# Kernel optimization log

Measured on AMD Instinct MI355X. Metric: run time of the kernel, lower is better.

## Reference

```python
import jax, jax.numpy as jnp
import numpy as np

EMBED_DIM = 1024
NUM_HEADS = 16
HEAD_DIM = EMBED_DIM // NUM_HEADS


def setup_inputs() -> dict:
    key = jax.random.key(0)
    ks = jax.random.split(key, 9)
    B, S, D = 2, 2048, EMBED_DIM
    scale = 1.0 / np.sqrt(D)
    x = jax.random.normal(ks[0], (B, S, D), dtype=jnp.float32)
    Wq = jax.random.normal(ks[1], (D, D), dtype=jnp.float32) * scale
    Wk = jax.random.normal(ks[2], (D, D), dtype=jnp.float32) * scale
    Wv = jax.random.normal(ks[3], (D, D), dtype=jnp.float32) * scale
    Wo = jax.random.normal(ks[4], (D, D), dtype=jnp.float32) * scale
    bq = jnp.zeros((D,), jnp.float32)
    bk = jnp.zeros((D,), jnp.float32)
    bv = jnp.zeros((D,), jnp.float32)
    bo = jnp.zeros((D,), jnp.float32)
    return {"x": x, "Wq": Wq, "bq": bq, "Wk": Wk, "bk": bk,
            "Wv": Wv, "bv": bv, "Wo": Wo, "bo": bo}


def reference(x, Wq, bq, Wk, bk, Wv, bv, Wo, bo):
    B, S, D = x.shape
    H, Dh = NUM_HEADS, HEAD_DIM
    # QKV projections -> [B, H, S, Dh]
    q = (x @ Wq + bq).reshape(B, S, H, Dh).transpose(0, 2, 1, 3)
    k = (x @ Wk + bk).reshape(B, S, H, Dh).transpose(0, 2, 1, 3)
    v = (x @ Wv + bv).reshape(B, S, H, Dh).transpose(0, 2, 1, 3)
    # scores [B, H, S, S], scaled by sqrt(head_dim)
    scores = jnp.einsum('bhqd,bhkd->bhqk', q, k) / jnp.sqrt(jnp.float32(Dh))
    attn = jax.nn.softmax(scores, axis=-1)
    out = jnp.einsum('bhqk,bhkd->bhqd', attn, v)  # [B, H, S, Dh]
    out = out.transpose(0, 2, 1, 3).reshape(B, S, D)
    return out @ Wo + bo
```

## Files before the change

### kernel.cpp

```cpp
#include <hip/hip_runtime.h>
#include <hip/hip_bf16.h>

typedef short bf16x8 __attribute__((ext_vector_type(8)));
typedef float f32x4 __attribute__((ext_vector_type(4)));

#define MFMA16(a, b, c) __builtin_amdgcn_mfma_f32_16x16x32_bf16((a), (b), (c), 0, 0, 0)

static constexpr int B_ = 2, S_ = 2048, D_ = 1024, H_ = 16, DH = 64;
static constexpr int M_ = B_ * S_;
static constexpr int K_ = D_;

static __device__ __forceinline__ ushort f2bf(float f) {
    __hip_bfloat16 h = __float2bfloat16(f);
    return *reinterpret_cast<ushort*>(&h);
}

static __device__ __forceinline__ void gload16(const ushort* g, ushort* l) {
    __builtin_amdgcn_global_load_lds((const __attribute__((address_space(1))) void*)g,
                                     (__attribute__((address_space(3))) void*)l, 16, 0, 0);
}

__global__ __launch_bounds__(256) void cvt_f2b(const float* __restrict__ in,
                                               ushort* __restrict__ out) {
    int i = blockIdx.x * blockDim.x + threadIdx.x;
    float4 v = reinterpret_cast<const float4*>(in)[i];
    ushort4 o;
    o.x = f2bf(v.x); o.y = f2bf(v.y); o.z = f2bf(v.z); o.w = f2bf(v.w);
    reinterpret_cast<ushort4*>(out)[i] = o;
}

__global__ __launch_bounds__(256) void transpose_w4(const float* __restrict__ W0,
                                                    const float* __restrict__ W1,
                                                    const float* __restrict__ W2,
                                                    const float* __restrict__ W3,
                                                    ushort* __restrict__ T0,
                                                    ushort* __restrict__ T1,
                                                    ushort* __restrict__ T2,
                                                    ushort* __restrict__ T3) {
    __shared__ float tile[32][33];
    int z = blockIdx.z;
    const float* W = (z == 0) ? W0 : (z == 1) ? W1 : (z == 2) ? W2 : W3;
    ushort* T = (z == 0) ? T0 : (z == 1) ? T1 : (z == 2) ? T2 : T3;
    int bx = blockIdx.x, by = blockIdx.y;
    int tx = threadIdx.x, ty = threadIdx.y;
#pragma unroll
    for (int i = 0; i < 4; i++)
        tile[ty + i * 8][tx] = W[(by * 32 + ty + i * 8) * D_ + bx * 32 + tx];
    __syncthreads();
#pragma unroll
    for (int i = 0; i < 4; i++)
        T[(bx * 32 + ty + i * 8) * K_ + by * 32 + tx] = f2bf(tile[tx][ty + i * 8]);
}

template <int MODE, int TN>
__global__ __launch_bounds__(256, 3) void gemm128(const ushort* __restrict__ A,
                                                  const ushort* __restrict__ Wt,
                                                  const float* __restrict__ bias_q,
                                                  const float* __restrict__ bias_k,
                                                  const float* __restrict__ bias_v,
                                                  ushort* __restrict__ Qb,
                                                  ushort* __restrict__ Kb,
                                                  ushort* __restrict__ Vtb,
                                                  float* __restrict__ outf) {
    constexpr int NJ = TN / 32;
    __shared__ __align__(16) ushort As[128 * 32];
    __shared__ __align__(16) ushort Bs[TN * 32];

    int m0 = blockIdx.x * 128;
    int n0 = blockIdx.y * TN;
    int t = threadIdx.x;
    int lane = t & 63, w = t >> 6;
    int ln = lane & 15, lq = lane >> 4;
    int wm = (w >> 1) * 64, wn = (w & 1) * (TN / 2);

    int c0 = t, c1 = t + 256;
    const ushort* Ag0 = A + (size_t)(m0 + (c0 >> 2)) * K_ + (c0 & 3) * 8;
    const ushort* Ag1 = A + (size_t)(m0 + (c1 >> 2)) * K_ + (c1 & 3) * 8;
    const ushort* Bg0 = Wt + (size_t)(n0 + (c0 >> 2)) * K_ + (c0 & 3) * 8;
    const ushort* Bg1 = Wt + (size_t)(n0 + (c1 >> 2)) * K_ + (c1 & 3) * 8;
    ushort* Al0 = As + c0 * 8;
    ushort* Al1 = As + c1 * 8;
    ushort* Bl0 = Bs + c0 * 8;
    ushort* Bl1 = Bs + c1 * 8;

    f32x4 acc[4][NJ];
#pragma unroll
    for (int i = 0; i < 4; i++)
#pragma unroll
        for (int j = 0; j < NJ; j++) acc[i][j] = f32x4{0.f, 0.f, 0.f, 0.f};

    for (int k0 = 0; k0 < K_; k0 += 32) {
        gload16(Ag0 + k0, Al0);
        gload16(Ag1 + k0, Al1);
        gload16(Bg0 + k0, Bl0);
        if (TN == 128) gload16(Bg1 + k0, Bl1);
        __syncthreads();
        bf16x8 af[4], bfr[NJ];
#pragma unroll
        for (int i = 0; i < 4; i++)
            af[i] = *reinterpret_cast<const bf16x8*>(As + (wm + i * 16 + ln) * 32 + lq * 8);
#pragma unroll
        for (int j = 0; j < NJ; j++)
            bfr[j] = *reinterpret_cast<const bf16x8*>(Bs + (wn + j * 16 + ln) * 32 + lq * 8);
#pragma unroll
        for (int i = 0; i < 4; i++)
#pragma unroll
            for (int j = 0; j < NJ; j++)
                acc[i][j] = MFMA16(af[i], bfr[j], acc[i][j]);
        __syncthreads();
    }

#pragma unroll
    for (int j = 0; j < NJ; j++) {
        int n = n0 + wn + j * 16 + ln;
        if (MODE == 1) {
            float bv = bias_q[n];
#pragma unroll
            for (int i = 0; i < 4; i++) {
#pragma unroll
                for (int r = 0; r < 4; r++) {
                    int m = m0 + wm + i * 16 + lq * 4 + r;
                    outf[(size_t)m * D_ + n] = acc[i][j][r] + bv;
                }
            }
        } else {
            int which = n >> 10, nn = n & 1023, h = nn >> 6, dh = nn & 63;
            const float* bp = (which == 0) ? bias_q : (which == 1) ? bias_k : bias_v;
            float bv = bp[nn];
            if (which == 2) {
#pragma unroll
                for (int i = 0; i < 4; i++) {
                    int m = m0 + wm + i * 16 + lq * 4;
                    int b = m >> 11, s0 = m & 2047;
                    ushort4 o4;
                    o4.x = f2bf(acc[i][j][0] + bv);
                    o4.y = f2bf(acc[i][j][1] + bv);
                    o4.z = f2bf(acc[i][j][2] + bv);
                    o4.w = f2bf(acc[i][j][3] + bv);
                    *reinterpret_cast<ushort4*>(Vtb + (((size_t)(b * H_ + h) * DH) + dh) * S_ + s0) = o4;
                }
            } else {
                ushort* dst = (which == 0) ? Qb : Kb;
#pragma unroll
                for (int i = 0; i < 4; i++) {
#pragma unroll
                    for (int r = 0; r < 4; r++) {
                        int m = m0 + wm + i * 16 + lq * 4 + r;
                        int b = m >> 11, s = m & 2047;
                        dst[(((b * H_ + h) * S_) + s) * DH + dh] = f2bf(acc[i][j][r] + bv);
                    }
                }
            }
        }
    }
}

__global__ __launch_bounds__(256, 4) void attn32d(const ushort* __restrict__ Q,
                                                  const ushort* __restrict__ K,
                                                  const ushort* __restrict__ Vt,
                                                  ushort* __restrict__ O) {
    __shared__ __align__(16) ushort Kl[2][2048];
    __shared__ __align__(16) ushort Vl[2][2048];
    __shared__ __align__(16) short Pl[4][16 * 36];

    int bid = blockIdx.x;
    int qb = bid & 31;
    int bh = bid >> 5;
    int t = threadIdx.x;
    int lane = t & 63, w = t >> 6;
    int ln = lane & 15, lq = lane >> 4;
    int qt = qb * 4 + w;

    const ushort* Qp = Q + (size_t)bh * S_ * DH;
    const ushort* Kp = K + (size_t)bh * S_ * DH;
    const ushort* Vp = Vt + (size_t)bh * DH * S_;

    bf16x8 qf0 = *reinterpret_cast<const bf16x8*>(Qp + (qt * 16 + ln) * DH + lq * 8);
    bf16x8 qf1 = *reinterpret_cast<const bf16x8*>(Qp + (qt * 16 + ln) * DH + 32 + lq * 8);

    const ushort* Kg = Kp + (size_t)(t & 31) * DH + (t >> 5) * 8;
    const ushort* Vg = Vp + (size_t)(t & 63) * S_ + (t >> 6) * 8;

    f32x4 o_acc[4];
    float l_part[4] = {0.f, 0.f, 0.f, 0.f};
#pragma unroll
    for (int nt = 0; nt < 4; nt++) o_acc[nt] = f32x4{0.f, 0.f, 0.f, 0.f};

    gload16(Kg, Kl[0] + t * 8);
    gload16(Vg, Vl[0] + t * 8);

    const float kSc = 0.18033688011112042f;

    for (int kt = 0; kt < S_ / 32; kt++) {
        __syncthreads();
        int cur = kt & 1;
        if (kt + 1 < S_ / 32) {
            int kb = (kt + 1) * 32;
            gload16(Kg + (size_t)kb * DH, Kl[cur ^ 1] + t * 8);
            gload16(Vg + kb, Vl[cur ^ 1] + t * 8);
        }
        const ushort* Kc = Kl[cur];
        const ushort* Vc = Vl[cur];

        f32x4 sc[2];
#pragma unroll
        for (int nt = 0; nt < 2; nt++) {
            bf16x8 kf0 = *reinterpret_cast<const bf16x8*>(Kc + (lq * 32 + nt * 16 + ln) * 8);
            bf16x8 kf1 = *reinterpret_cast<const bf16x8*>(Kc + ((4 + lq) * 32 + nt * 16 + ln) * 8);
            f32x4 c = {0.f, 0.f, 0.f, 0.f};
            c = MFMA16(qf0, kf0, c);
            c = MFMA16(qf1, kf1, c);
            sc[nt] = c;
        }
#pragma unroll
        for (int nt = 0; nt < 2; nt++)
#pragma unroll
            for (int r = 0; r < 4; r++) {
                float p = exp2f(sc[nt][r] * kSc);
                l_part[r] += p;
                Pl[w][(lq * 4 + r) * 36 + nt * 16 + ln] = (short)f2bf(p);
            }
        bf16x8 pf = *reinterpret_cast<const bf16x8*>(&Pl[w][ln * 36 + lq * 8]);
#pragma unroll
        for (int nt = 0; nt < 4; nt++) {
            bf16x8 vf = *reinterpret_cast<const bf16x8*>(Vc + (lq * 64 + nt * 16 + ln) * 8);
            o_acc[nt] = MFMA16(pf, vf, o_acc[nt]);
        }
    }

    float linv[4];
#pragma unroll
    for (int r = 0; r < 4; r++) {
        float l = l_part[r];
#pragma unroll
        for (int d = 1; d < 16; d <<= 1) l += __shfl_xor(l, d, 64);
        linv[r] = 1.0f / l;
    }
    int b = bh >> 4, h = bh & 15;
#pragma unroll
    for (int nt = 0; nt < 4; nt++)
#pragma unroll
        for (int r = 0; r < 4; r++) {
            int s = qt * 16 + lq * 4 + r;
            O[((b * S_ + s) * H_ + h) * DH + nt * 16 + ln] =
                f2bf(o_acc[nt][r] * linv[r]);
        }
}

extern "C" void kernel_launch(void* const* d_in, const int* in_sizes, int n_in,
                              void* d_out, int out_size, void* d_ws, size_t ws_size,
                              hipStream_t stream) {
    const float* x  = (const float*)d_in[0];
    const float* Wq = (const float*)d_in[1];
    const float* bq = (const float*)d_in[2];
    const float* Wk = (const float*)d_in[3];
    const float* bk = (const float*)d_in[4];
    const float* Wv = (const float*)d_in[5];
    const float* bv = (const float*)d_in[6];
    const float* Wo = (const float*)d_in[7];
    const float* bo = (const float*)d_in[8];
    float* out = (float*)d_out;

    char* ws = (char*)d_ws;
    const size_t MB = 1024 * 1024;
    ushort* wtq = (ushort*)(ws + 0 * MB);
    ushort* wtk = (ushort*)(ws + 2 * MB);
    ushort* wtv = (ushort*)(ws + 4 * MB);
    ushort* wto = (ushort*)(ws + 6 * MB);
    ushort* xb  = (ushort*)(ws + 8 * MB);
    ushort* Qb  = (ushort*)(ws + 16 * MB);
    ushort* Kb  = (ushort*)(ws + 24 * MB);
    ushort* Vtb = (ushort*)(ws + 32 * MB);
    ushort* AO  = (ushort*)(ws + 40 * MB);

    cvt_f2b<<<(M_ * K_ / 4) / 256, 256, 0, stream>>>(x, xb);

    transpose_w4<<<dim3(32, 32, 4), dim3(32, 8), 0, stream>>>(
        Wq, Wk, Wv, Wo, wtq, wtk, wtv, wto);

    gemm128<0, 128><<<dim3(M_ / 128, 3072 / 128), 256, 0, stream>>>(
        xb, wtq, bq, bk, bv, Qb, Kb, Vtb, nullptr);

    attn32d<<<32 * 32, 256, 0, stream>>>(Qb, Kb, Vtb, AO);

    gemm128<1, 64><<<dim3(M_ / 128, D_ / 64), 256, 0, stream>>>(
        AO, wto, bo, nullptr, nullptr, nullptr, nullptr, nullptr, out);
}
```

Measured before the change: 214.6 us.

## Split attention over two key halves and merge partial outputs in a combine kernel

The attention kernel now launches twice as many blocks, each covering half of the keys. Each block writes a normalized partial output plus its row sum, and a new combine kernel merges the two halves weighted by those sums. The softmax scale (with log2e folded in) is also moved into the Q weights and bias so the inner loop skips one multiply. This trades an extra kernel launch, partial-output traffic and an extra bf16 rounding for more parallelism in the attention stage. There is still no max subtraction, so it relies on scores staying small enough for exp2 not to overflow.

```diff
diff --git a/kernel.cpp b/kernel.cpp
--- a/kernel.cpp
+++ b/kernel.cpp
@@ -9,10 +9,16 @@
 static constexpr int B_ = 2, S_ = 2048, D_ = 1024, H_ = 16, DH = 64;
 static constexpr int M_ = B_ * S_;
 static constexpr int K_ = D_;
+static constexpr float kQS = 0.18033688011112042f;
 
 static __device__ __forceinline__ ushort f2bf(float f) {
     __hip_bfloat16 h = __float2bfloat16(f);
     return *reinterpret_cast<ushort*>(&h);
+}
+static __device__ __forceinline__ float bf2f(ushort u) {
+    __hip_bfloat16 h;
+    *reinterpret_cast<ushort*>(&h) = u;
+    return __bfloat162float(h);
 }
 
 static __device__ __forceinline__ void gload16(const ushort* g, ushort* l) {
@@ -41,6 +47,7 @@
     int z = blockIdx.z;
     const float* W = (z == 0) ? W0 : (z == 1) ? W1 : (z == 2) ? W2 : W3;
     ushort* T = (z == 0) ? T0 : (z == 1) ? T1 : (z == 2) ? T2 : T3;
+    float sc = (z == 0) ? kQS : 1.0f;
     int bx = blockIdx.x, by = blockIdx.y;
     int tx = threadIdx.x, ty = threadIdx.y;
 #pragma unroll
@@ -49,7 +56,7 @@
     __syncthreads();
 #pragma unroll
     for (int i = 0; i < 4; i++)
-        T[(bx * 32 + ty + i * 8) * K_ + by * 32 + tx] = f2bf(tile[tx][ty + i * 8]);
+        T[(bx * 32 + ty + i * 8) * K_ + by * 32 + tx] = f2bf(tile[tx][ty + i * 8] * sc);
 }
 
 template <int MODE, int TN>
@@ -127,6 +134,7 @@
             int which = n >> 10, nn = n & 1023, h = nn >> 6, dh = nn & 63;
             const float* bp = (which == 0) ? bias_q : (which == 1) ? bias_k : bias_v;
             float bv = bp[nn];
+            if (which == 0) bv *= kQS;
             if (which == 2) {
 #pragma unroll
                 for (int i = 0; i < 4; i++) {
@@ -158,22 +166,26 @@
 __global__ __launch_bounds__(256, 4) void attn32d(const ushort* __restrict__ Q,
                                                   const ushort* __restrict__ K,
                                                   const ushort* __restrict__ Vt,
-                                                  ushort* __restrict__ O) {
+                                                  ushort* __restrict__ O1,
+                                                  ushort* __restrict__ O2,
+                                                  float* __restrict__ L) {
     __shared__ __align__(16) ushort Kl[2][2048];
     __shared__ __align__(16) ushort Vl[2][2048];
     __shared__ __align__(16) short Pl[4][16 * 36];
 
     int bid = blockIdx.x;
-    int qb = bid & 31;
-    int bh = bid >> 5;
+    int half = bid >> 10;
+    int rem = bid & 1023;
+    int qb = rem & 31;
+    int bh = rem >> 5;
     int t = threadIdx.x;
     int lane = t & 63, w = t >> 6;
     int ln = lane & 15, lq = lane >> 4;
     int qt = qb * 4 + w;
 
     const ushort* Qp = Q + (size_t)bh * S_ * DH;
-    const ushort* Kp = K + (size_t)bh * S_ * DH;
-    const ushort* Vp = Vt + (size_t)bh * DH * S_;
+    const ushort* Kp = K + (size_t)bh * S_ * DH + (size_t)half * 1024 * DH;
+    const ushort* Vp = Vt + (size_t)bh * DH * S_ + (size_t)half * 1024;
 
     bf16x8 qf0 = *reinterpret_cast<const bf16x8*>(Qp + (qt * 16 + ln) * DH + lq * 8);
     bf16x8 qf1 = *reinterpret_cast<const bf16x8*>(Qp + (qt * 16 + ln) * DH + 32 + lq * 8);
@@ -189,12 +201,10 @@
     gload16(Kg, Kl[0] + t * 8);
     gload16(Vg, Vl[0] + t * 8);
 
-    const float kSc = 0.18033688011112042f;
-
-    for (int kt = 0; kt < S_ / 32; kt++) {
+    for (int kt = 0; kt < 32; kt++) {
         __syncthreads();
         int cur = kt & 1;
-        if (kt + 1 < S_ / 32) {
+        if (kt + 1 < 32) {
             int kb = (kt + 1) * 32;
             gload16(Kg + (size_t)kb * DH, Kl[cur ^ 1] + t * 8);
             gload16(Vg + kb, Vl[cur ^ 1] + t * 8);
@@ -216,7 +226,7 @@
         for (int nt = 0; nt < 2; nt++)
 #pragma unroll
             for (int r = 0; r < 4; r++) {
-                float p = exp2f(sc[nt][r] * kSc);
+                float p = exp2f(sc[nt][r]);
                 l_part[r] += p;
                 Pl[w][(lq * 4 + r) * 36 + nt * 16 + ln] = (short)f2bf(p);
             }
@@ -228,6 +238,8 @@
         }
     }
 
+    ushort* Op = half ? O2 : O1;
+    float* Lp = L + ((size_t)half * 32 + bh) * S_;
     float linv[4];
 #pragma unroll
     for (int r = 0; r < 4; r++) {
@@ -235,6 +247,7 @@
 #pragma unroll
         for (int d = 1; d < 16; d <<= 1) l += __shfl_xor(l, d, 64);
         linv[r] = 1.0f / l;
+        if (ln == 0) Lp[qt * 16 + lq * 4 + r] = l;
     }
     int b = bh >> 4, h = bh & 15;
 #pragma unroll
@@ -242,9 +255,41 @@
 #pragma unroll
         for (int r = 0; r < 4; r++) {
             int s = qt * 16 + lq * 4 + r;
-            O[((b * S_ + s) * H_ + h) * DH + nt * 16 + ln] =
+            Op[((b * S_ + s) * H_ + h) * DH + nt * 16 + ln] =
                 f2bf(o_acc[nt][r] * linv[r]);
         }
+}
+
+__global__ __launch_bounds__(256) void attn_comb(const ushort* __restrict__ O1,
+                                                 const ushort* __restrict__ O2,
+                                                 const float* __restrict__ L,
+                                                 ushort* __restrict__ AO) {
+    int i = blockIdx.x * 256 + threadIdx.x;
+    int row = i >> 7;
+    int col = (i & 127) * 8;
+    int h = col >> 6;
+    int b = row >> 11, s = row & 2047;
+    int bh = b * 16 + h;
+    float l1 = L[(size_t)bh * S_ + s];
+    float l2 = L[((size_t)32 + bh) * S_ + s];
+    float inv = 1.0f / (l1 + l2);
+    float w1 = l1 * inv, w2 = l2 * inv;
+    size_t off = (size_t)row * D_ + col;
+    ushort4 a0 = reinterpret_cast<const ushort4*>(O1 + off)[0];
+    ushort4 a1 = reinterpret_cast<const ushort4*>(O1 + off)[1];
+    ushort4 b0 = reinterpret_cast<const ushort4*>(O2 + off)[0];
+    ushort4 b1 = reinterpret_cast<const ushort4*>(O2 + off)[1];
+    ushort4 o0, o1v;
+    o0.x = f2bf(w1 * bf2f(a0.x) + w2 * bf2f(b0.x));
+    o0.y = f2bf(w1 * bf2f(a0.y) + w2 * bf2f(b0.y));
+    o0.z = f2bf(w1 * bf2f(a0.z) + w2 * bf2f(b0.z));
+    o0.w = f2bf(w1 * bf2f(a0.w) + w2 * bf2f(b0.w));
+    o1v.x = f2bf(w1 * bf2f(a1.x) + w2 * bf2f(b1.x));
+    o1v.y = f2bf(w1 * bf2f(a1.y) + w2 * bf2f(b1.y));
+    o1v.z = f2bf(w1 * bf2f(a1.z) + w2 * bf2f(b1.z));
+    o1v.w = f2bf(w1 * bf2f(a1.w) + w2 * bf2f(b1.w));
+    reinterpret_cast<ushort4*>(AO + off)[0] = o0;
+    reinterpret_cast<ushort4*>(AO + off)[1] = o1v;
 }
 
 extern "C" void kernel_launch(void* const* d_in, const int* in_sizes, int n_in,
@@ -272,6 +317,9 @@
     ushort* Kb  = (ushort*)(ws + 24 * MB);
     ushort* Vtb = (ushort*)(ws + 32 * MB);
     ushort* AO  = (ushort*)(ws + 40 * MB);
+    ushort* O1  = (ushort*)(ws + 8 * MB);
+    ushort* O2  = (ushort*)(ws + 48 * MB);
+    float*  Lw  = (float*)(ws + 56 * MB);
 
     cvt_f2b<<<(M_ * K_ / 4) / 256, 256, 0, stream>>>(x, xb);
 
@@ -281,7 +329,8 @@
     gemm128<0, 128><<<dim3(M_ / 128, 3072 / 128), 256, 0, stream>>>(
         xb, wtq, bq, bk, bv, Qb, Kb, Vtb, nullptr);
 
-    attn32d<<<32 * 32, 256, 0, stream>>>(Qb, Kb, Vtb, AO);
+    attn32d<<<2048, 256, 0, stream>>>(Qb, Kb, Vtb, O1, O2, Lw);
+    attn_comb<<<(M_ * D_ / 8) / 256, 256, 0, stream>>>(O1, O2, Lw, AO);
 
     gemm128<1, 64><<<dim3(M_ / 128, D_ / 64), 256, 0, stream>>>(
         AO, wto, bo, nullptr, nullptr, nullptr, nullptr, nullptr, out);
```

Result: slower. 229.4 us (+6.9%).

## Fold softmax scale into Q weights and use 64-key single-buffered attention tiles

Applied to the files above, without the earlier changes.

Pre-multiplies Wq and bq by the log2e/sqrt(dh) factor during the weight transpose, so the attention loop can call exp2 on raw scores. Replaces the double-buffered 32-key attention loop with a 64-key tile loop that loads K/V into a single LDS buffer, with a barrier before and after compute. This halves the iteration count and amortizes barriers and P staging, but gives up prefetch overlap of the next tile with compute and drops the explicit occupancy hint.

```diff
diff --git a/kernel.cpp b/kernel.cpp
--- a/kernel.cpp
+++ b/kernel.cpp
@@ -9,6 +9,7 @@
 static constexpr int B_ = 2, S_ = 2048, D_ = 1024, H_ = 16, DH = 64;
 static constexpr int M_ = B_ * S_;
 static constexpr int K_ = D_;
+static constexpr float kQS = 0.18033688011112042f;
 
 static __device__ __forceinline__ ushort f2bf(float f) {
     __hip_bfloat16 h = __float2bfloat16(f);
@@ -41,6 +42,7 @@
     int z = blockIdx.z;
     const float* W = (z == 0) ? W0 : (z == 1) ? W1 : (z == 2) ? W2 : W3;
     ushort* T = (z == 0) ? T0 : (z == 1) ? T1 : (z == 2) ? T2 : T3;
+    float sc = (z == 0) ? kQS : 1.0f;
     int bx = blockIdx.x, by = blockIdx.y;
     int tx = threadIdx.x, ty = threadIdx.y;
 #pragma unroll
@@ -49,7 +51,7 @@
     __syncthreads();
 #pragma unroll
     for (int i = 0; i < 4; i++)
-        T[(bx * 32 + ty + i * 8) * K_ + by * 32 + tx] = f2bf(tile[tx][ty + i * 8]);
+        T[(bx * 32 + ty + i * 8) * K_ + by * 32 + tx] = f2bf(tile[tx][ty + i * 8] * sc);
 }
 
 template <int MODE, int TN>
@@ -127,6 +129,7 @@
             int which = n >> 10, nn = n & 1023, h = nn >> 6, dh = nn & 63;
             const float* bp = (which == 0) ? bias_q : (which == 1) ? bias_k : bias_v;
             float bv = bp[nn];
+            if (which == 0) bv *= kQS;
             if (which == 2) {
 #pragma unroll
                 for (int i = 0; i < 4; i++) {
@@ -155,13 +158,13 @@
     }
 }
 
-__global__ __launch_bounds__(256, 4) void attn32d(const ushort* __restrict__ Q,
-                                                  const ushort* __restrict__ K,
-                                                  const ushort* __restrict__ Vt,
-                                                  ushort* __restrict__ O) {
-    __shared__ __align__(16) ushort Kl[2][2048];
-    __shared__ __align__(16) ushort Vl[2][2048];
-    __shared__ __align__(16) short Pl[4][16 * 36];
+__global__ __launch_bounds__(256) void attn64r(const ushort* __restrict__ Q,
+                                               const ushort* __restrict__ K,
+                                               const ushort* __restrict__ Vt,
+                                               ushort* __restrict__ O) {
+    __shared__ __align__(16) ushort Kl[512 * 8];
+    __shared__ __align__(16) ushort Vl[512 * 8];
+    __shared__ __align__(16) ushort Pl[4][16 * 72];
 
     int bid = blockIdx.x;
     int qb = bid & 31;
@@ -178,54 +181,57 @@
     bf16x8 qf0 = *reinterpret_cast<const bf16x8*>(Qp + (qt * 16 + ln) * DH + lq * 8);
     bf16x8 qf1 = *reinterpret_cast<const bf16x8*>(Qp + (qt * 16 + ln) * DH + 32 + lq * 8);
 
-    const ushort* Kg = Kp + (size_t)(t & 31) * DH + (t >> 5) * 8;
-    const ushort* Vg = Vp + (size_t)(t & 63) * S_ + (t >> 6) * 8;
+    int c0 = t, c1 = t + 256;
+    const ushort* Kg0 = Kp + (size_t)(c0 & 63) * DH + (c0 >> 6) * 8;
+    const ushort* Kg1 = Kp + (size_t)(c1 & 63) * DH + (c1 >> 6) * 8;
+    const ushort* Vg0 = Vp + (size_t)(c0 & 63) * S_ + (c0 >> 6) * 8;
+    const ushort* Vg1 = Vp + (size_t)(c1 & 63) * S_ + (c1 >> 6) * 8;
+    ushort* Kl0 = Kl + c0 * 8;
+    ushort* Kl1 = Kl + c1 * 8;
+    ushort* Vl0 = Vl + c0 * 8;
+    ushort* Vl1 = Vl + c1 * 8;
 
     f32x4 o_acc[4];
     float l_part[4] = {0.f, 0.f, 0.f, 0.f};
 #pragma unroll
     for (int nt = 0; nt < 4; nt++) o_acc[nt] = f32x4{0.f, 0.f, 0.f, 0.f};
 
-    gload16(Kg, Kl[0] + t * 8);
-    gload16(Vg, Vl[0] + t * 8);
-
-    const float kSc = 0.18033688011112042f;
-
-    for (int kt = 0; kt < S_ / 32; kt++) {
-        __syncthreads();
-        int cur = kt & 1;
-        if (kt + 1 < S_ / 32) {
-            int kb = (kt + 1) * 32;
-            gload16(Kg + (size_t)kb * DH, Kl[cur ^ 1] + t * 8);
-            gload16(Vg + kb, Vl[cur ^ 1] + t * 8);
-        }
-        const ushort* Kc = Kl[cur];
-        const ushort* Vc = Vl[cur];
-
-        f32x4 sc[2];
-#pragma unroll
-        for (int nt = 0; nt < 2; nt++) {
-            bf16x8 kf0 = *reinterpret_cast<const bf16x8*>(Kc + (lq * 32 + nt * 16 + ln) * 8);
-            bf16x8 kf1 = *reinterpret_cast<const bf16x8*>(Kc + ((4 + lq) * 32 + nt * 16 + ln) * 8);
+    for (int kt = 0; kt < S_ / 64; kt++) {
+        int kb = kt * 64;
+        gload16(Kg0 + (size_t)kb * DH, Kl0);
+        gload16(Kg1 + (size_t)kb * DH, Kl1);
+        gload16(Vg0 + kb, Vl0);
+        gload16(Vg1 + kb, Vl1);
+        __syncthreads();
+
+        f32x4 sc[4];
+#pragma unroll
+        for (int nt = 0; nt < 4; nt++) {
+            bf16x8 kf0 = *reinterpret_cast<const bf16x8*>(Kl + (lq * 64 + nt * 16 + ln) * 8);
+            bf16x8 kf1 = *reinterpret_cast<const bf16x8*>(Kl + ((4 + lq) * 64 + nt * 16 + ln) * 8);
             f32x4 c = {0.f, 0.f, 0.f, 0.f};
             c = MFMA16(qf0, kf0, c);
             c = MFMA16(qf1, kf1, c);
             sc[nt] = c;
         }
 #pragma unroll
-        for (int nt = 0; nt < 2; nt++)
+        for (int nt = 0; nt < 4; nt++)
 #pragma unroll
             for (int r = 0; r < 4; r++) {
-                float p = exp2f(sc[nt][r] * kSc);
+                float p = exp2f(sc[nt][r]);
                 l_part[r] += p;
-                Pl[w][(lq * 4 + r) * 36 + nt * 16 + ln] = (short)f2bf(p);
+                Pl[w][(lq * 4 + r) * 72 + nt * 16 + ln] = f2bf(p);
             }
-        bf16x8 pf = *reinterpret_cast<const bf16x8*>(&Pl[w][ln * 36 + lq * 8]);
+        bf16x8 pf0 = *reinterpret_cast<const bf16x8*>(&Pl[w][ln * 72 + lq * 8]);
+        bf16x8 pf1 = *reinterpret_cast<const bf16x8*>(&Pl[w][ln * 72 + 32 + lq * 8]);
 #pragma unroll
         for (int nt = 0; nt < 4; nt++) {
-            bf16x8 vf = *reinterpret_cast<const bf16x8*>(Vc + (lq * 64 + nt * 16 + ln) * 8);
-            o_acc[nt] = MFMA16(pf, vf, o_acc[nt]);
-        }
+            bf16x8 vf0 = *reinterpret_cast<const bf16x8*>(Vl + (lq * 64 + nt * 16 + ln) * 8);
+            bf16x8 vf1 = *reinterpret_cast<const bf16x8*>(Vl + ((4 + lq) * 64 + nt * 16 + ln) * 8);
+            o_acc[nt] = MFMA16(pf0, vf0, o_acc[nt]);
+            o_acc[nt] = MFMA16(pf1, vf1, o_acc[nt]);
+        }
+        __syncthreads();
     }
 
     float linv[4];
@@ -281,7 +287,7 @@
     gemm128<0, 128><<<dim3(M_ / 128, 3072 / 128), 256, 0, stream>>>(
         xb, wtq, bq, bk, bv, Qb, Kb, Vtb, nullptr);
 
-    attn32d<<<32 * 32, 256, 0, stream>>>(Qb, Kb, Vtb, AO);
+    attn64r<<<32 * 32, 256, 0, stream>>>(Qb, Kb, Vtb, AO);
 
     gemm128<1, 64><<<dim3(M_ / 128, D_ / 64), 256, 0, stream>>>(
         AO, wto, bo, nullptr, nullptr, nullptr, nullptr, nullptr, out);
```

After: 207.6 us. 3.3% less time.
